# Kernel tuning notes

Hardware: AMD Instinct MI355X
Metric: run time of the kernel (lower is better)

Reference implementation:

```python
import jax, jax.numpy as jnp
import numpy as np

H = 4
HD = 32
C = 128
NU = 40000
NI = 40000
E = 200000


def _linear(x, W, b):
    # torch Linear: y = x @ W.T + b, W is [out, in]
    return x @ W.T + b


def _counts_in(query, sorted_keys):
    l = jnp.searchsorted(sorted_keys, query, side='left')
    r = jnp.searchsorted(sorted_keys, query, side='right')
    return (r - l).astype(jnp.float32)


def _segment_softmax(scores, seg, n):
    # scores: [E, H], seg: [E] destination ids
    m = jax.ops.segment_max(scores, seg, num_segments=n)
    m = jnp.where(jnp.isfinite(m), m, 0.0)
    e = jnp.exp(scores - m[seg])
    z = jax.ops.segment_sum(e, seg, num_segments=n)
    return e / z[seg]


def _deg_count(idx, n):
    return jnp.zeros((n,), jnp.float32).at[idx].add(1.0)


def _layernorm(x):
    mu = x.mean(-1, keepdims=True)
    var = ((x - mu) ** 2).mean(-1, keepdims=True)
    return (x - mu) / jnp.sqrt(var + 1e-5)


def _relation(x_src, x_dst, src, dst, t_src, t_dst,
              Wq, bq, Wk, bk, Wv, bv, Wo, bo,
              head_bias, beta, tau_raw, gamma, delta,
              counts, recips, n_dst):
    Q = _linear(x_dst, Wq, bq).reshape(-1, H, HD)
    K = _linear(x_src, Wk, bk).reshape(-1, H, HD)
    V = _linear(x_src, Wv, bv).reshape(-1, H, HD)
    Qe, Ke, Ve = Q[dst], K[src], V[src]                      # [E, H, HD]
    scores = (Qe * Ke).sum(-1) / jnp.sqrt(jnp.float32(HD))   # [E, H]
    scores = scores + head_bias
    dt = jnp.abs(t_dst[dst] - t_src[src]) + 1e-6
    tau = jax.nn.softplus(tau_raw) + 1e-6
    scores = scores + (-jnp.log1p(dt / tau))[:, None] * beta
    scores = scores + jnp.log1p(counts)[:, None] * gamma
    scores = scores + recips[:, None] * delta
    w = _segment_softmax(scores, dst, n_dst)                 # [E, H]
    out_e = (Ve * w[:, :, None]).reshape(-1, C)
    out_e = _linear(out_e, Wo, bo)
    return jnp.zeros((n_dst, C), x_dst.dtype).at[dst].add(out_e)


def setup_inputs() -> dict:
    key = jax.random.key(0)
    ks = jax.random.split(key, 20)
    inp = {
        'x_user': jax.random.normal(ks[0], (NU, C), jnp.float32),
        'x_item': jax.random.normal(ks[1], (NI, C), jnp.float32),
        't_user': jax.random.uniform(ks[2], (NU,), jnp.float32) * 100.0,
        't_item': jax.random.uniform(ks[3], (NI,), jnp.float32) * 100.0,
        'edge_index_ui': jax.random.randint(ks[4], (2, E), 0, NU, jnp.int32),
        'edge_index_iu': jax.random.randint(ks[5], (2, E), 0, NI, jnp.int32),
        'Wq': jax.random.normal(ks[6], (C, C), jnp.float32) * 0.05,
        'bq': jax.random.normal(ks[7], (C,), jnp.float32) * 0.05,
        'Wk': jax.random.normal(ks[8], (C, C), jnp.float32) * 0.05,
        'bk': jax.random.normal(ks[9], (C,), jnp.float32) * 0.05,
        'Wv': jax.random.normal(ks[10], (C, C), jnp.float32) * 0.05,
        'bv': jax.random.normal(ks[11], (C,), jnp.float32) * 0.05,
        'Wo': jax.random.normal(ks[12], (C, C), jnp.float32) * 0.05,
        'bo': jax.random.normal(ks[13], (C,), jnp.float32) * 0.05,
        'rel_head_bias': jax.random.normal(ks[14], (2, H), jnp.float32) * 0.1,
        'time_beta': jax.random.normal(ks[15], (2, H), jnp.float32) * 0.1,
        'time_tau_raw': jax.random.normal(ks[16], (2,), jnp.float32),
        'gamma_multirel': jax.random.normal(ks[17], (2, H), jnp.float32) * 0.1,
        'delta_recip': jax.random.normal(ks[18], (2, H), jnp.float32) * 0.1,
    }
    return inp


def reference(x_user, x_item, t_user, t_item, edge_index_ui, edge_index_iu,
              Wq, bq, Wk, bk, Wv, bv, Wo, bo,
              rel_head_bias, time_beta, time_tau_raw, gamma_multirel, delta_recip):
    su, du = edge_index_ui[0], edge_index_ui[1]   # user -> item
    si, di = edge_index_iu[0], edge_index_iu[1]   # item -> user
    # multirel counts (pair multiplicity - 1) and reciprocity flags, per relation
    pid_ui = su * NI + du            # (user,item) pair ids (fits int32: NU*NI < 2^31)
    pid_iu = si * NU + di            # (item,user) pair ids
    rev_for_ui = di * NI + si        # reversed pairs of iu edges in (user,item) space
    rev_for_iu = du * NU + su        # reversed pairs of ui edges in (item,user) space
    counts_ui = _counts_in(pid_ui, jnp.sort(pid_ui)) - 1.0
    counts_iu = _counts_in(pid_iu, jnp.sort(pid_iu)) - 1.0
    recips_ui = (_counts_in(pid_ui, jnp.sort(rev_for_ui)) > 0).astype(jnp.float32)
    recips_iu = (_counts_in(pid_iu, jnp.sort(rev_for_iu)) > 0).astype(jnp.float32)

    out_item = _relation(x_user, x_item, su, du, t_user, t_item,
                         Wq, bq, Wk, bk, Wv, bv, Wo, bo,
                         rel_head_bias[0], time_beta[0], time_tau_raw[0],
                         gamma_multirel[0], delta_recip[0], counts_ui, recips_ui, NI)
    out_user = _relation(x_item, x_user, si, di, t_item, t_user,
                         Wq, bq, Wk, bk, Wv, bv, Wo, bo,
                         rel_head_bias[1], time_beta[1], time_tau_raw[1],
                         gamma_multirel[1], delta_recip[1], counts_iu, recips_iu, NU)
    # degree centrality bias: total (in + out) degree added to every channel
    deg_user = _deg_count(su, NU) + _deg_count(di, NU)
    deg_item = _deg_count(du, NI) + _deg_count(si, NI)
    out_user = out_user + deg_user[:, None]
    out_item = out_item + deg_item[:, None]
    return _layernorm(out_user + x_user), _layernorm(out_item + x_item)
```

## Files before the change

### kernel.cpp

```cpp
#include <hip/hip_runtime.h>
#include <math.h>

constexpr int kH  = 4;
constexpr int kHD = 32;
constexpr int kC  = 128;
constexpr int kNU = 40000;
constexpr int kNI = 40000;
constexpr int kE  = 200000;
constexpr int kNT = kNU + kNI;
constexpr int kSB = (kNT + 1023) / 1024;
constexpr int kTilesPerSide = kNU / 16;
constexpr int kTiles = kNT / 16;
constexpr int kGemmBlocks  = 768;
constexpr int kTableBlocks = 1536;
constexpr int kFusedBlocks = 2304;

#define DEV_INLINE __device__ __forceinline__

typedef short bf16x8 __attribute__((ext_vector_type(8)));
typedef float f32x4  __attribute__((ext_vector_type(4)));
typedef uint32_t u32x4 __attribute__((ext_vector_type(4)));
typedef unsigned long long u64;

DEV_INLINE unsigned short f2bf(float f) {
  uint32_t u = __float_as_uint(f);
  u += 0x7fffu + ((u >> 16) & 1u);
  return (unsigned short)(u >> 16);
}

DEV_INLINE float bflo(uint32_t u) { return __uint_as_float(u << 16); }
DEV_INLINE float bfhi(uint32_t u) { return __uint_as_float(u & 0xffff0000u); }

DEV_INLINE int swz(int row, int elem) {
  return (elem & 7) | (((elem >> 3) ^ (row & 7)) << 3);
}

DEV_INLINE int rpf(const int* __restrict__ rp, const int* __restrict__ boff, int i) {
  return rp[i] + boff[i >> 10];
}

__global__ void cast4w_bf16(const float* __restrict__ w0, const float* __restrict__ w1,
                            const float* __restrict__ w2, const float* __restrict__ w3,
                            unsigned short* __restrict__ o0, unsigned short* __restrict__ o1,
                            unsigned short* __restrict__ o2, unsigned short* __restrict__ o3) {
  int i = blockIdx.x * blockDim.x + threadIdx.x;
  int m = i >> 12, j = i & 4095;
  const float* in = (m == 0) ? w0 : (m == 1) ? w1 : (m == 2) ? w2 : w3;
  unsigned short* out = (m == 0) ? o0 : (m == 1) ? o1 : (m == 2) ? o2 : o3;
  float4 v = ((const float4*)in)[j];
  ushort4 o = {f2bf(v.x), f2bf(v.y), f2bf(v.z), f2bf(v.w)};
  ((ushort4*)out)[j] = o;
}

__global__ __launch_bounds__(256, 3) void qkv_build(
    const float* __restrict__ Xu, const float* __restrict__ Xi,
    const unsigned short* __restrict__ Wq, const unsigned short* __restrict__ Wk,
    const unsigned short* __restrict__ Wv,
    const float* __restrict__ bq, const float* __restrict__ bk,
    const float* __restrict__ bv,
    unsigned short* __restrict__ Qu, unsigned short* __restrict__ Ku,
    unsigned short* __restrict__ Vu,
    unsigned short* __restrict__ Qi, unsigned short* __restrict__ Ki,
    unsigned short* __restrict__ Vi,
    const int* __restrict__ du, const int* __restrict__ di,
    int* __restrict__ deg_all, int* __restrict__ pos_all) {
  __shared__ unsigned short sx[16 * kC];
  __shared__ unsigned short sr[3 * 16 * kC];
  const int bid = blockIdx.x;
  const int tid = threadIdx.x;

  if (bid % 3 != 1) {
    const int tb = (bid / 3) * 2 + ((bid % 3) ? 1 : 0);
    for (int t = tb * 256 + tid; t < 2 * kE; t += kTableBlocks * 256) {
      if (t < kE) {
        pos_all[t] = atomicAdd(&deg_all[du[t]], 1);
      } else {
        pos_all[t] = atomicAdd(&deg_all[kNI + di[t - kE]], 1);
      }
    }
    return;
  }

  const int gb   = bid / 3;
  const int wave = tid >> 6;
  const int lane = tid & 63;
  const int mr   = lane & 15;
  const int quad = lane >> 4;
  const int ct0  = wave * 2;
  const int srow = tid >> 4;
  const int schk = tid & 15;

  bf16x8 wf[3][2][4];
  {
    const unsigned short* Ws[3] = {Wq, Wk, Wv};
#pragma unroll
    for (int m = 0; m < 3; ++m)
#pragma unroll
      for (int c = 0; c < 2; ++c) {
        const unsigned short* wrow = Ws[m] + (size_t)((ct0 + c) * 16 + mr) * kC + quad * 8;
#pragma unroll
        for (int kc = 0; kc < 4; ++kc) wf[m][c][kc] = *(const bf16x8*)(wrow + kc * 32);
      }
  }

  int tile = gb;
  float4 xa, xb;
  {
    const bool item = tile >= kTilesPerSide;
    const float* X = item ? Xi : Xu;
    const int base = (item ? tile - kTilesPerSide : tile) * 16;
    const float* xr = X + (size_t)(base + srow) * kC + schk * 8;
    xa = ((const float4*)xr)[0];
    xb = ((const float4*)xr)[1];
  }

  for (; tile < kTiles; tile += kGemmBlocks) {
    const bool item = tile >= kTilesPerSide;
    const int base = (item ? tile - kTilesPerSide : tile) * 16;

    {
      bf16x8 p;
      p[0] = (short)f2bf(xa.x); p[1] = (short)f2bf(xa.y);
      p[2] = (short)f2bf(xa.z); p[3] = (short)f2bf(xa.w);
      p[4] = (short)f2bf(xb.x); p[5] = (short)f2bf(xb.y);
      p[6] = (short)f2bf(xb.z); p[7] = (short)f2bf(xb.w);
      *(bf16x8*)(sx + srow * kC + ((schk ^ (srow & 7)) << 3)) = p;
    }
    __syncthreads();

    bf16x8 b[4];
#pragma unroll
    for (int kc = 0; kc < 4; ++kc)
      b[kc] = *(const bf16x8*)(sx + mr * kC + (((quad + kc * 4) ^ (mr & 7)) << 3));

    int ntile = tile + kGemmBlocks;
    if (ntile < kTiles) {
      const bool nit = ntile >= kTilesPerSide;
      const float* X = nit ? Xi : Xu;
      const int nbase = (nit ? ntile - kTilesPerSide : ntile) * 16;
      const float* xr = X + (size_t)(nbase + srow) * kC + schk * 8;
      xa = ((const float4*)xr)[0];
      xb = ((const float4*)xr)[1];
    }

    f32x4 acc[3][2];
#pragma unroll
    for (int m = 0; m < 3; ++m) {
      acc[m][0] = (f32x4){0.f, 0.f, 0.f, 0.f};
      acc[m][1] = (f32x4){0.f, 0.f, 0.f, 0.f};
    }
#pragma unroll
    for (int kc = 0; kc < 4; ++kc)
#pragma unroll
      for (int m = 0; m < 3; ++m)
#pragma unroll
        for (int c = 0; c < 2; ++c)
          acc[m][c] = __builtin_amdgcn_mfma_f32_16x16x32_bf16(wf[m][c][kc], b[kc], acc[m][c], 0, 0, 0);

    const float* bs[3] = {bq, bk, bv};
#pragma unroll
    for (int m = 0; m < 3; ++m)
#pragma unroll
      for (int c = 0; c < 2; ++c) {
        int c0 = (ct0 + c) * 16 + quad * 4;
        float4 bb = *(const float4*)(bs[m] + c0);
        uint2 p;
        p.x = (uint32_t)f2bf(acc[m][c][0] + bb.x) | ((uint32_t)f2bf(acc[m][c][1] + bb.y) << 16);
        p.y = (uint32_t)f2bf(acc[m][c][2] + bb.z) | ((uint32_t)f2bf(acc[m][c][3] + bb.w) << 16);
        *(uint2*)(sr + (m * 16 + mr) * kC + swz(mr, c0)) = p;
      }
    __syncthreads();

    {
      unsigned short* Os[3] = {item ? Qi : Qu, item ? Ki : Ku, item ? Vi : Vu};
      const int el = (schk ^ (srow & 7)) << 3;
#pragma unroll
      for (int m = 0; m < 3; ++m) {
        bf16x8 v = *(const bf16x8*)(sr + (m * 16 + srow) * kC + el);
        *(bf16x8*)(Os[m] + (size_t)(base + srow) * kC + schk * 8) = v;
      }
    }
  }
}

__global__ __launch_bounds__(256) void scan1(const int* __restrict__ in,
                                             int* __restrict__ out,
                                             int* __restrict__ bsum, int n) {
  __shared__ int sh[256];
  const int t = threadIdx.x;
  const int base = blockIdx.x * 1024 + t * 4;
  int4 v = {0, 0, 0, 0};
  if (base + 3 < n) {
    v = *(const int4*)(in + base);
  } else {
    if (base + 0 < n) v.x = in[base + 0];
    if (base + 1 < n) v.y = in[base + 1];
    if (base + 2 < n) v.z = in[base + 2];
    if (base + 3 < n) v.w = in[base + 3];
  }
  int s = v.x + v.y + v.z + v.w;
  sh[t] = s;
  __syncthreads();
  int val = s;
  for (int off = 1; off < 256; off <<= 1) {
    int add = (t >= off) ? sh[t - off] : 0;
    __syncthreads();
    val += add;
    sh[t] = val;
    __syncthreads();
  }
  int excl = val - s;
  if (base + 0 < n) out[base + 0] = excl;
  if (base + 1 < n) out[base + 1] = excl + v.x;
  if (base + 2 < n) out[base + 2] = excl + v.x + v.y;
  if (base + 3 < n) out[base + 3] = excl + v.x + v.y + v.z;
  if (t == 255) bsum[blockIdx.x] = val;
}

__global__ __launch_bounds__(128) void scan2(const int* __restrict__ bsum,
                                             int* __restrict__ boff,
                                             int* __restrict__ rp_tail, int nb) {
  __shared__ int sh[128];
  const int t = threadIdx.x;
  int v = (t < nb) ? bsum[t] : 0;
  sh[t] = v;
  __syncthreads();
  int val = v;
  for (int off = 1; off < 128; off <<= 1) {
    int add = (t >= off) ? sh[t - off] : 0;
    __syncthreads();
    val += add;
    sh[t] = val;
    __syncthreads();
  }
  if (t < nb) boff[t] = val - v;
  if (t == nb - 1) *rp_tail = v;
}

__global__ void scatter_pk(const int* __restrict__ su, const int* __restrict__ du,
                           const int* __restrict__ si, const int* __restrict__ di,
                           const int* __restrict__ rp_all, const int* __restrict__ boff,
                           const int* __restrict__ pos_all,
                           u64* __restrict__ el_all) {
  int t = blockIdx.x * blockDim.x + threadIdx.x;
  if (t >= 2 * kE) return;
  int e, s, dg;
  if (t < kE) { e = t;       s = su[e]; dg = du[e]; }
  else        { e = t - kE;  s = si[e]; dg = kNI + di[e]; }
  el_all[rpf(rp_all, boff, dg) + pos_all[t]] = (u64)(uint32_t)e | ((u64)(uint32_t)s << 32);
}

__global__ void bias_csr(const int* __restrict__ su, const int* __restrict__ du,
                         const int* __restrict__ si, const int* __restrict__ di,
                         const float* __restrict__ t_user, const float* __restrict__ t_item,
                         const int* __restrict__ rp_all, const int* __restrict__ boff,
                         const u64* __restrict__ el_all,
                         const float* __restrict__ hb, const float* __restrict__ beta,
                         const float* __restrict__ taur,
                         const float* __restrict__ gamma, const float* __restrict__ delta,
                         float4* __restrict__ bias_ui, float4* __restrict__ bias_iu) {
  int t = blockIdx.x * blockDim.x + threadIdx.x;
  if (t >= 2 * kE) return;
  const int rel = (t >= kE) ? 1 : 0;
  const int e = rel ? t - kE : t;
  int s, d; float ts, td; int dg, rg;
  if (rel == 0) {
    s = su[e]; d = du[e]; ts = t_user[s]; td = t_item[d];
    dg = d;
    rg = kNI + s;
  } else {
    s = si[e]; d = di[e]; ts = t_item[s]; td = t_user[d];
    dg = kNI + d;
    rg = s;
  }
  int b0 = rpf(rp_all, boff, dg), b1 = rpf(rp_all, boff, dg + 1);
  int cnt = 0;
  for (int p = b0; p < b1; ++p) cnt += ((int)(el_all[p] >> 32) == s);
  int r0 = rpf(rp_all, boff, rg), r1 = rpf(rp_all, boff, rg + 1);
  int rcp = 0;
  for (int p = r0; p < r1; ++p) rcp |= ((int)(el_all[p] >> 32) == d);

  float cntv = (float)(cnt - 1);
  float rec  = (float)rcp;
  float dt   = fabsf(td - ts) + 1e-6f;
  float tau  = log1pf(expf(taur[rel])) + 1e-6f;
  float tterm = -log1pf(dt / tau);
  float lc    = log1pf(cntv);
  const float* hp = hb + rel * kH;
  const float* bp = beta + rel * kH;
  const float* gp = gamma + rel * kH;
  const float* dp = delta + rel * kH;
  const float kL2E = 1.4426950408889634f;
  float4 b;
  b.x = (hp[0] + bp[0] * tterm + gp[0] * lc + dp[0] * rec) * kL2E;
  b.y = (hp[1] + bp[1] * tterm + gp[1] * lc + dp[1] * rec) * kL2E;
  b.z = (hp[2] + bp[2] * tterm + gp[2] * lc + dp[2] * rec) * kL2E;
  b.w = (hp[3] + bp[3] * tterm + gp[3] * lc + dp[3] * rec) * kL2E;
  (rel ? bias_iu : bias_ui)[e] = b;
}

__global__ __launch_bounds__(256) void attn_agg(
    const int* __restrict__ rp_all, const int* __restrict__ boff,
    const u64* __restrict__ el_all,
    const unsigned short* __restrict__ Qi, const unsigned short* __restrict__ Ku,
    const unsigned short* __restrict__ Vu,
    const unsigned short* __restrict__ Qu, const unsigned short* __restrict__ Ki,
    const unsigned short* __restrict__ Vi,
    const float* __restrict__ bias_ui, const float* __restrict__ bias_iu,
    unsigned short* __restrict__ h_ui, unsigned short* __restrict__ h_iu) {
  const int wave = threadIdx.x >> 6;
  const int lane = threadIdx.x & 63;
  const int grp  = lane >> 4;
  const int sub  = lane & 15;
  const int h    = sub >> 2;
  const int ch0  = h * kHD + (sub & 3) * 8;
  const int g = blockIdx.x * 4 + wave;
  if (g >= kNT) return;
  const bool isU = g >= kNI;
  const int n = isU ? g - kNI : g;
  const unsigned short* Q = isU ? Qu : Qi;
  const unsigned short* K = isU ? Ki : Ku;
  const unsigned short* V = isU ? Vi : Vu;
  const float* bias = isU ? bias_iu : bias_ui;
  unsigned short* out = isU ? h_iu : h_ui;

  const int beg = rpf(rp_all, boff, g), end = rpf(rp_all, boff, g + 1);
  const float kScaleL2E = 1.4426950408889634f * 0.17677669529663687f;

  float qf[8];
  {
    u32x4 qv = *(const u32x4*)(Q + (size_t)n * kC + ch0);
#pragma unroll
    for (int w = 0; w < 4; ++w) { qf[2 * w] = bflo(qv[w]); qf[2 * w + 1] = bfhi(qv[w]); }
  }

  float z = 0.f;
  float acc[8] = {0.f, 0.f, 0.f, 0.f, 0.f, 0.f, 0.f, 0.f};

  const int p0 = beg + grp;
  int eA = 0, sA = 0;
  if (p0 < end) { u64 pk = el_all[p0]; eA = (int)pk; sA = (int)(pk >> 32); }
  int eB = 0, sB = 0;
  if (p0 + 4 < end) { u64 pk = el_all[p0 + 4]; eB = (int)pk; sB = (int)(pk >> 32); }
  u32x4 kA = *(const u32x4*)(K + (size_t)sA * kC + ch0);
  u32x4 vA = *(const u32x4*)(V + (size_t)sA * kC + ch0);
  float bA = bias[eA * 4 + h];

  for (int p = p0; p < end; p += 4) {
    u32x4 kB = *(const u32x4*)(K + (size_t)sB * kC + ch0);
    u32x4 vB = *(const u32x4*)(V + (size_t)sB * kC + ch0);
    float bB = bias[eB * 4 + h];
    int eC = 0, sC = 0;
    if (p + 8 < end) { u64 pk = el_all[p + 8]; eC = (int)pk; sC = (int)(pk >> 32); }

    float d0 = qf[0] * bflo(kA[0]);
    float d1 = qf[1] * bfhi(kA[0]);
    d0 = fmaf(qf[2], bflo(kA[1]), d0);
    d1 = fmaf(qf[3], bfhi(kA[1]), d1);
    d0 = fmaf(qf[4], bflo(kA[2]), d0);
    d1 = fmaf(qf[5], bfhi(kA[2]), d1);
    d0 = fmaf(qf[6], bflo(kA[3]), d0);
    d1 = fmaf(qf[7], bfhi(kA[3]), d1);
    float dsc = d0 + d1;
    dsc += __shfl_xor(dsc, 1);
    dsc += __shfl_xor(dsc, 2);
    float wgt = __builtin_amdgcn_exp2f(fmaf(dsc, kScaleL2E, bA));
    z += wgt;
#pragma unroll
    for (int w = 0; w < 4; ++w) {
      acc[2 * w]     = fmaf(bflo(vA[w]), wgt, acc[2 * w]);
      acc[2 * w + 1] = fmaf(bfhi(vA[w]), wgt, acc[2 * w + 1]);
    }
    kA = kB; vA = vB; bA = bB; eB = eC; sB = sC;
  }

#pragma unroll
  for (int j = 0; j < 8; ++j) {
    acc[j] += __shfl_xor(acc[j], 16);
    acc[j] += __shfl_xor(acc[j], 32);
  }
  z += __shfl_xor(z, 16);
  z += __shfl_xor(z, 32);

  const float zi = (end > beg) ? 1.0f / z : 0.0f;
  if (grp == 0) {
    bf16x8 o;
#pragma unroll
    for (int j = 0; j < 8; ++j) o[j] = (short)f2bf(acc[j] * zi);
    *(bf16x8*)(out + (size_t)n * kC + ch0) = o;
  }
}

__global__ __launch_bounds__(256, 4) void wo_ln(
    const unsigned short* __restrict__ Hiu, const unsigned short* __restrict__ Hui,
    const unsigned short* __restrict__ Wo,
    const float* __restrict__ Xu, const float* __restrict__ Xi,
    const int* __restrict__ degU, const int* __restrict__ degI,
    const float* __restrict__ bo, float* __restrict__ out) {
  __shared__ unsigned short sh_h[16 * kC];
  __shared__ float sh_p[64 * 2];
  const int tid  = threadIdx.x;
  const int wave = tid >> 6;
  const int lane = tid & 63;
  const int mr   = lane & 15;
  const int quad = lane >> 4;
  const int ct0  = wave * 2;
  const int srow = tid >> 4;
  const int schk = tid & 15;

  bf16x8 wf[2][4];
#pragma unroll
  for (int c = 0; c < 2; ++c) {
    const unsigned short* wrow = Wo + (size_t)((ct0 + c) * 16 + mr) * kC + quad * 8;
#pragma unroll
    for (int kc = 0; kc < 4; ++kc) wf[c][kc] = *(const bf16x8*)(wrow + kc * 32);
  }
  float4 bb[2];
  bb[0] = *(const float4*)(bo + ct0 * 16 + quad * 4);
  bb[1] = *(const float4*)(bo + (ct0 + 1) * 16 + quad * 4);

  int tile = blockIdx.x;
  bf16x8 hv;
  {
    const bool item = tile >= kTilesPerSide;
    const unsigned short* Hs = item ? Hui : Hiu;
    const int base = (item ? tile - kTilesPerSide : tile) * 16;
    hv = *(const bf16x8*)(Hs + (size_t)(base + srow) * kC + schk * 8);
  }

  for (; tile < kTiles; tile += gridDim.x) {
    const bool item = tile >= kTilesPerSide;
    const int base = (item ? tile - kTilesPerSide : tile) * 16;

    *(bf16x8*)(sh_h + srow * kC + ((schk ^ (srow & 7)) << 3)) = hv;
    __syncthreads();

    bf16x8 b[4];
#pragma unroll
    for (int kc = 0; kc < 4; ++kc)
      b[kc] = *(const bf16x8*)(sh_h + mr * kC + (((quad + kc * 4) ^ (mr & 7)) << 3));

    int ntile = tile + gridDim.x;
    if (ntile < kTiles) {
      const bool nit = ntile >= kTilesPerSide;
      const unsigned short* Hs = nit ? Hui : Hiu;
      const int nbase = (nit ? ntile - kTilesPerSide : ntile) * 16;
      hv = *(const bf16x8*)(Hs + (size_t)(nbase + srow) * kC + schk * 8);
    }

    f32x4 acc[2];
    acc[0] = (f32x4){0.f, 0.f, 0.f, 0.f};
    acc[1] = (f32x4){0.f, 0.f, 0.f, 0.f};
#pragma unroll
    for (int kc = 0; kc < 4; ++kc) {
      acc[0] = __builtin_amdgcn_mfma_f32_16x16x32_bf16(wf[0][kc], b[kc], acc[0], 0, 0, 0);
      acc[1] = __builtin_amdgcn_mfma_f32_16x16x32_bf16(wf[1][kc], b[kc], acc[1], 0, 0, 0);
    }

    const int n = base + mr;
    const float* Xs = item ? Xi : Xu;
    const float fdg = (float)(item ? degI[n] : degU[n]);
    float y[8], s1 = 0.f, s2 = 0.f;
#pragma unroll
    for (int c = 0; c < 2; ++c) {
      int c0 = (ct0 + c) * 16 + quad * 4;
      float4 xv = *(const float4*)(Xs + (size_t)n * kC + c0);
      y[c * 4 + 0] = acc[c][0] + xv.x + fdg * bb[c].x;
      y[c * 4 + 1] = acc[c][1] + xv.y + fdg * bb[c].y;
      y[c * 4 + 2] = acc[c][2] + xv.z + fdg * bb[c].z;
      y[c * 4 + 3] = acc[c][3] + xv.w + fdg * bb[c].w;
#pragma unroll
      for (int j = 0; j < 4; ++j) {
        s1 += y[c * 4 + j];
        s2 += y[c * 4 + j] * y[c * 4 + j];
      }
    }
    s1 += __shfl_xor(s1, 16); s2 += __shfl_xor(s2, 16);
    s1 += __shfl_xor(s1, 32); s2 += __shfl_xor(s2, 32);
    if (quad == 0) {
      sh_p[(wave * 16 + mr) * 2]     = s1;
      sh_p[(wave * 16 + mr) * 2 + 1] = s2;
    }
    __syncthreads();
    float t1 = 0.f, t2 = 0.f;
#pragma unroll
    for (int ww = 0; ww < 4; ++ww) {
      t1 += sh_p[(ww * 16 + mr) * 2];
      t2 += sh_p[(ww * 16 + mr) * 2 + 1];
    }
    float mu   = t1 * (1.0f / 128.0f);
    float var  = t2 * (1.0f / 128.0f) - mu * mu;
    float rstd = rsqrtf(fmaxf(var, 0.0f) + 1e-5f);
    float* op = out + (item ? (size_t)kNU * kC : (size_t)0) + (size_t)n * kC;
#pragma unroll
    for (int c = 0; c < 2; ++c) {
      int c0 = (ct0 + c) * 16 + quad * 4;
      float4 o = {(y[c * 4 + 0] - mu) * rstd, (y[c * 4 + 1] - mu) * rstd,
                  (y[c * 4 + 2] - mu) * rstd, (y[c * 4 + 3] - mu) * rstd};
      *(float4*)(op + c0) = o;
    }
  }
}

extern "C" void kernel_launch(void* const* d_in, const int* in_sizes, int n_in,
                              void* d_out, int out_size, void* d_ws, size_t ws_size,
                              hipStream_t stream) {
  const float* x_user = (const float*)d_in[0];
  const float* x_item = (const float*)d_in[1];
  const float* t_user = (const float*)d_in[2];
  const float* t_item = (const float*)d_in[3];
  const int*   eui    = (const int*)d_in[4];
  const int*   eiu    = (const int*)d_in[5];
  const float* Wq = (const float*)d_in[6];
  const float* bq = (const float*)d_in[7];
  const float* Wk = (const float*)d_in[8];
  const float* bk = (const float*)d_in[9];
  const float* Wv = (const float*)d_in[10];
  const float* bv = (const float*)d_in[11];
  const float* Wo = (const float*)d_in[12];
  const float* bo = (const float*)d_in[13];
  const float* hb    = (const float*)d_in[14];
  const float* beta  = (const float*)d_in[15];
  const float* taur  = (const float*)d_in[16];
  const float* gamma = (const float*)d_in[17];
  const float* delta = (const float*)d_in[18];

  const int* su = eui;       const int* du = eui + kE;
  const int* si = eiu;       const int* di = eiu + kE;

  float* w = (float*)d_ws;
  size_t o = 0;
  unsigned short* qu_b = (unsigned short*)(w + o); o += (size_t)kNU * kC / 2;
  unsigned short* ku_b = (unsigned short*)(w + o); o += (size_t)kNU * kC / 2;
  unsigned short* vu_b = (unsigned short*)(w + o); o += (size_t)kNU * kC / 2;
  unsigned short* qi_b = (unsigned short*)(w + o); o += (size_t)kNI * kC / 2;
  unsigned short* ki_b = (unsigned short*)(w + o); o += (size_t)kNI * kC / 2;
  unsigned short* vi_b = (unsigned short*)(w + o); o += (size_t)kNI * kC / 2;
  unsigned short* h_ui = (unsigned short*)(w + o); o += (size_t)kNI * kC / 2;
  unsigned short* h_iu = (unsigned short*)(w + o); o += (size_t)kNU * kC / 2;
  unsigned short* wq_b = (unsigned short*)(w + o); o += kC * kC / 2;
  unsigned short* wk_b = (unsigned short*)(w + o); o += kC * kC / 2;
  unsigned short* wv_b = (unsigned short*)(w + o); o += kC * kC / 2;
  unsigned short* wo_b = (unsigned short*)(w + o); o += kC * kC / 2;
  float* zero_base = w + o;
  int* deg_all = (int*)(w + o); o += kNT;
  size_t zero_bytes = (size_t)((w + o) - zero_base) * sizeof(float);
  float* bias_ui = w + o; o += (size_t)kE * kH;
  float* bias_iu = w + o; o += (size_t)kE * kH;
  int* rp_all  = (int*)(w + o); o += kNT + 1;
  int* bsum    = (int*)(w + o); o += kSB;
  int* boff    = (int*)(w + o); o += kSB;
  o = (o + 1) & ~(size_t)1;
  u64* el_all  = (u64*)(w + o); o += (size_t)2 * kE * 2;
  int* pos_all = (int*)h_ui;

  hipMemsetAsync(zero_base, 0, zero_bytes, stream);

  dim3 b256(256);
  cast4w_bf16<<<(4 * kC * kC / 4) / 256, b256, 0, stream>>>(Wq, Wk, Wv, Wo,
                                                            wq_b, wk_b, wv_b, wo_b);

  qkv_build<<<kFusedBlocks, b256, 0, stream>>>(
      x_user, x_item, wq_b, wk_b, wv_b, bq, bk, bv,
      qu_b, ku_b, vu_b, qi_b, ki_b, vi_b,
      du, di, deg_all, pos_all);

  scan1<<<kSB, b256, 0, stream>>>(deg_all, rp_all, bsum, kNT);
  scan2<<<1, dim3(128), 0, stream>>>(bsum, boff, rp_all + kNT, kSB);

  int g2E = (2 * kE + 255) / 256;
  scatter_pk<<<g2E, b256, 0, stream>>>(su, du, si, di, rp_all, boff, pos_all, el_all);

  bias_csr<<<g2E, b256, 0, stream>>>(su, du, si, di, t_user, t_item,
                                     rp_all, boff, el_all,
                                     hb, beta, taur, gamma, delta,
                                     (float4*)bias_ui, (float4*)bias_iu);

  attn_agg<<<kNT / 4, b256, 0, stream>>>(rp_all, boff, el_all,
                                         qi_b, ku_b, vu_b, qu_b, ki_b, vi_b,
                                         bias_ui, bias_iu, h_ui, h_iu);

  wo_ln<<<768, b256, 0, stream>>>(h_iu, h_ui, wo_b, x_user, x_item,
                                  deg_all + kNI, deg_all, bo, (float*)d_out);
}
```

Baseline: 254.5 us.

## Map one 16-lane group per destination node in attention aggregation

The attention aggregation kernel now gives each destination node 16 lanes instead of a full 64-lane wave. Each group walks its edges one at a time with one-step prefetch, so the cross-group shuffle reduction goes away. Four times as many nodes are processed per block, which cuts idle lanes when nodes have few edges (average degree is about 5). In exchange, each node's edge loop is serial over 16 lanes, so per-node latency grows and load imbalance within a wave depends on degree variance.

```diff
diff --git a/kernel.cpp b/kernel.cpp
--- a/kernel.cpp
+++ b/kernel.cpp
@@ -308,13 +308,11 @@
     const unsigned short* __restrict__ Vi,
     const float* __restrict__ bias_ui, const float* __restrict__ bias_iu,
     unsigned short* __restrict__ h_ui, unsigned short* __restrict__ h_iu) {
-  const int wave = threadIdx.x >> 6;
-  const int lane = threadIdx.x & 63;
-  const int grp  = lane >> 4;
-  const int sub  = lane & 15;
-  const int h    = sub >> 2;
-  const int ch0  = h * kHD + (sub & 3) * 8;
-  const int g = blockIdx.x * 4 + wave;
+  const int tid = threadIdx.x;
+  const int sub = tid & 15;
+  const int h   = sub >> 2;
+  const int ch0 = h * kHD + (sub & 3) * 8;
+  const int g = blockIdx.x * 16 + (tid >> 4);
   if (g >= kNT) return;
   const bool isU = g >= kNI;
   const int n = isU ? g - kNI : g;
@@ -337,58 +335,45 @@
   float z = 0.f;
   float acc[8] = {0.f, 0.f, 0.f, 0.f, 0.f, 0.f, 0.f, 0.f};
 
-  const int p0 = beg + grp;
-  int eA = 0, sA = 0;
-  if (p0 < end) { u64 pk = el_all[p0]; eA = (int)pk; sA = (int)(pk >> 32); }
-  int eB = 0, sB = 0;
-  if (p0 + 4 < end) { u64 pk = el_all[p0 + 4]; eB = (int)pk; sB = (int)(pk >> 32); }
-  u32x4 kA = *(const u32x4*)(K + (size_t)sA * kC + ch0);
-  u32x4 vA = *(const u32x4*)(V + (size_t)sA * kC + ch0);
-  float bA = bias[eA * 4 + h];
-
-  for (int p = p0; p < end; p += 4) {
-    u32x4 kB = *(const u32x4*)(K + (size_t)sB * kC + ch0);
-    u32x4 vB = *(const u32x4*)(V + (size_t)sB * kC + ch0);
-    float bB = bias[eB * 4 + h];
-    int eC = 0, sC = 0;
-    if (p + 8 < end) { u64 pk = el_all[p + 8]; eC = (int)pk; sC = (int)(pk >> 32); }
-
-    float d0 = qf[0] * bflo(kA[0]);
-    float d1 = qf[1] * bfhi(kA[0]);
-    d0 = fmaf(qf[2], bflo(kA[1]), d0);
-    d1 = fmaf(qf[3], bfhi(kA[1]), d1);
-    d0 = fmaf(qf[4], bflo(kA[2]), d0);
-    d1 = fmaf(qf[5], bfhi(kA[2]), d1);
-    d0 = fmaf(qf[6], bflo(kA[3]), d0);
-    d1 = fmaf(qf[7], bfhi(kA[3]), d1);
+  int e0 = 0, s0 = 0;
+  if (beg < end) { u64 pk = el_all[beg]; e0 = (int)pk; s0 = (int)(pk >> 32); }
+  u32x4 k0 = *(const u32x4*)(K + (size_t)s0 * kC + ch0);
+  u32x4 v0 = *(const u32x4*)(V + (size_t)s0 * kC + ch0);
+  float b0 = bias[e0 * 4 + h];
+
+  for (int p = beg; p < end; ++p) {
+    int e1 = 0, s1 = 0;
+    if (p + 1 < end) { u64 pk = el_all[p + 1]; e1 = (int)pk; s1 = (int)(pk >> 32); }
+    u32x4 k1 = *(const u32x4*)(K + (size_t)s1 * kC + ch0);
+    u32x4 v1 = *(const u32x4*)(V + (size_t)s1 * kC + ch0);
+    float b1 = bias[e1 * 4 + h];
+
+    float d0 = qf[0] * bflo(k0[0]);
+    float d1 = qf[1] * bfhi(k0[0]);
+    d0 = fmaf(qf[2], bflo(k0[1]), d0);
+    d1 = fmaf(qf[3], bfhi(k0[1]), d1);
+    d0 = fmaf(qf[4], bflo(k0[2]), d0);
+    d1 = fmaf(qf[5], bfhi(k0[2]), d1);
+    d0 = fmaf(qf[6], bflo(k0[3]), d0);
+    d1 = fmaf(qf[7], bfhi(k0[3]), d1);
     float dsc = d0 + d1;
     dsc += __shfl_xor(dsc, 1);
     dsc += __shfl_xor(dsc, 2);
-    float wgt = __builtin_amdgcn_exp2f(fmaf(dsc, kScaleL2E, bA));
+    float wgt = __builtin_amdgcn_exp2f(fmaf(dsc, kScaleL2E, b0));
     z += wgt;
 #pragma unroll
     for (int w = 0; w < 4; ++w) {
-      acc[2 * w]     = fmaf(bflo(vA[w]), wgt, acc[2 * w]);
-      acc[2 * w + 1] = fmaf(bfhi(vA[w]), wgt, acc[2 * w + 1]);
-    }
-    kA = kB; vA = vB; bA = bB; eB = eC; sB = sC;
-  }
-
-#pragma unroll
-  for (int j = 0; j < 8; ++j) {
-    acc[j] += __shfl_xor(acc[j], 16);
-    acc[j] += __shfl_xor(acc[j], 32);
-  }
-  z += __shfl_xor(z, 16);
-  z += __shfl_xor(z, 32);
+      acc[2 * w]     = fmaf(bflo(v0[w]), wgt, acc[2 * w]);
+      acc[2 * w + 1] = fmaf(bfhi(v0[w]), wgt, acc[2 * w + 1]);
+    }
+    k0 = k1; v0 = v1; b0 = b1;
+  }
 
   const float zi = (end > beg) ? 1.0f / z : 0.0f;
-  if (grp == 0) {
-    bf16x8 o;
-#pragma unroll
-    for (int j = 0; j < 8; ++j) o[j] = (short)f2bf(acc[j] * zi);
-    *(bf16x8*)(out + (size_t)n * kC + ch0) = o;
-  }
+  bf16x8 o;
+#pragma unroll
+  for (int j = 0; j < 8; ++j) o[j] = (short)f2bf(acc[j] * zi);
+  *(bf16x8*)(out + (size_t)n * kC + ch0) = o;
 }
 
 __global__ __launch_bounds__(256, 4) void wo_ln(
@@ -576,9 +561,9 @@
                                      hb, beta, taur, gamma, delta,
                                      (float4*)bias_ui, (float4*)bias_iu);
 
-  attn_agg<<<kNT / 4, b256, 0, stream>>>(rp_all, boff, el_all,
-                                         qi_b, ku_b, vu_b, qu_b, ki_b, vi_b,
-                                         bias_ui, bias_iu, h_ui, h_iu);
+  attn_agg<<<(kNT + 15) / 16, b256, 0, stream>>>(rp_all, boff, el_all,
+                                                 qi_b, ku_b, vu_b, qu_b, ki_b, vi_b,
+                                                 bias_ui, bias_iu, h_ui, h_iu);
 
   wo_ln<<<768, b256, 0, stream>>>(h_iu, h_ui, wo_b, x_user, x_item,
                                   deg_all + kNI, deg_all, bo, (float*)d_out);
```

Result: no change. 255.0 us (+0.2%).
